# Kernel optimization log

Hardware: AMD Instinct MI355X
Metric: run time of the kernel (lower is better)

The kernel has to match this reference:

```python
import jax, jax.numpy as jnp
import numpy as np

DIM = 384
HEADS = 6
HEAD_DIM = DIM // HEADS
SCALE = HEAD_DIM ** -0.5
B = 16
HW = 56
NUM_TOKENS = 49


def _layernorm(x, g, b, eps):
    m = x.mean(-1, keepdims=True)
    v = ((x - m) ** 2).mean(-1, keepdims=True)
    return (x - m) * jax.lax.rsqrt(v + eps) * g + b


def _avgpool2(x):  # [B,C,H,W] -> [B,C,H/2,W/2], AvgPool2d(2,2)
    Bx, C, H, W = x.shape
    return x.reshape(Bx, C, H // 2, 2, W // 2, 2).mean(axis=(3, 5))


def _mha(q, k, v):  # q [B,Nq,C], k/v [B,Nk,C] -> [B,Nq,C]
    Bx, Nq, C = q.shape
    Nk = k.shape[1]
    qh = q.reshape(Bx, Nq, HEADS, HEAD_DIM).transpose(0, 2, 1, 3) * SCALE
    kh = k.reshape(Bx, Nk, HEADS, HEAD_DIM).transpose(0, 2, 1, 3)
    vh = v.reshape(Bx, Nk, HEADS, HEAD_DIM).transpose(0, 2, 1, 3)
    attn = jax.nn.softmax(jnp.einsum('bhqd,bhkd->bhqk', qh, kh), axis=-1)
    out = jnp.einsum('bhqk,bhkd->bhqd', attn, vh)
    return out.transpose(0, 2, 1, 3).reshape(Bx, Nq, C)


def setup_inputs() -> dict:
    key = jax.random.key(0)
    ks = jax.random.split(key, 16)
    s = 0.02
    return {
        'x': jax.random.normal(ks[0], (B, HW * HW, DIM), jnp.float32),
        'global_token': jax.random.normal(ks[1], (B, NUM_TOKENS, DIM), jnp.float32),
        # ConvEncoder (wsas[0]) params; linear weights stored [in,out] (= torch W.T)
        'we_dw_w': jax.random.normal(ks[2], (DIM, 1, 3, 3), jnp.float32) * 0.1,
        'we_dw_b': jnp.zeros((DIM,), jnp.float32),
        'we_ln_g': jnp.ones((DIM,), jnp.float32),
        'we_ln_b': jnp.zeros((DIM,), jnp.float32),
        'we_pw1_w': jax.random.normal(ks[3], (DIM, 4 * DIM), jnp.float32) * s,
        'we_pw1_b': jnp.zeros((4 * DIM,), jnp.float32),
        'we_pw2_w': jax.random.normal(ks[4], (4 * DIM, DIM), jnp.float32) * s,
        'we_pw2_b': jnp.zeros((DIM,), jnp.float32),
        'we_gamma': jnp.full((DIM,), 1e-6, jnp.float32),
        # ConvBNReLU (wsas[1]) params
        'cb_conv_w': jax.random.normal(ks[5], (DIM, DIM, 3, 3), jnp.float32) * s,
        'cb_ln_g': jnp.ones((DIM,), jnp.float32),
        'cb_ln_b': jnp.zeros((DIM,), jnp.float32),
        # attention projections (qkv_bias=False)
        'ga_qkv_w': jax.random.normal(ks[6], (DIM, 3 * DIM), jnp.float32) * s,
        'ug_kv_w': jax.random.normal(ks[7], (DIM, 2 * DIM), jnp.float32) * s,
        'ug_q_w': jax.random.normal(ks[8], (DIM, DIM), jnp.float32) * s,
        'gb_kv_w': jax.random.normal(ks[9], (DIM, 2 * DIM), jnp.float32) * s,
        'gb_q_w': jax.random.normal(ks[10], (DIM, DIM), jnp.float32) * s,
        'proj_w': jax.random.normal(ks[11], (DIM, DIM), jnp.float32) * s,
        'proj_b': jnp.zeros((DIM,), jnp.float32),
        'H': HW,
        'W': HW,
    }


def reference(x, global_token, we_dw_w, we_dw_b, we_ln_g, we_ln_b, we_pw1_w, we_pw1_b, we_pw2_w, we_pw2_b, we_gamma, cb_conv_w, cb_ln_g, cb_ln_b, ga_qkv_w, ug_kv_w, ug_q_w, gb_kv_w, gb_q_w, proj_w, proj_b, H, W):
    Bx, N, C = x.shape
    x_origin = x
    xc = x.reshape(Bx, H, W, C).transpose(0, 3, 1, 2)  # NCHW
    res = xc
    y = jax.lax.conv_general_dilated(xc, we_dw_w, (1, 1), 'SAME', feature_group_count=C, dimension_numbers=('NCHW', 'OIHW', 'NCHW')) + we_dw_b[None, :, None, None]
    y = y.transpose(0, 2, 3, 1)  # NHWC
    y = _layernorm(y, we_ln_g, we_ln_b, 1e-6)
    y = jax.nn.gelu(y @ we_pw1_w + we_pw1_b, approximate=False)
    y = (y @ we_pw2_w + we_pw2_b) * we_gamma
    xc = res + y.transpose(0, 3, 1, 2)
    x_local = xc.reshape(Bx, C, N).transpose(0, 2, 1)  # multi-scale[0]
    xc = _avgpool2(xc)  # down_1
    # --- wsas[1]: ConvBNReLU (3x3 conv, no bias + LN + ReLU) ---
    y = jax.lax.conv_general_dilated(xc, cb_conv_w, (1, 1), 'SAME', dimension_numbers=('NCHW', 'OIHW', 'NCHW'))
    y = _layernorm(y.transpose(0, 2, 3, 1), cb_ln_g, cb_ln_b, 1e-5)
    xc = jax.nn.relu(y).transpose(0, 3, 1, 2)
    xc = _avgpool2(xc)  # down_2 -> [B,C,14,14]
    xd = xc.reshape(Bx, C, -1).transpose(0, 2, 1)  # [B,196,C]
    # --- global aggregation: MHSA over downsampled tokens ---
    q, k, v = jnp.split(xd @ ga_qkv_w, 3, axis=-1)
    x_ds = _mha(q, k, v)
    # --- global token update: q = global tokens, kv = downsampled tokens ---
    k2, v2 = jnp.split(x_ds @ ug_kv_w, 2, axis=-1)
    gt = _mha(global_token @ ug_q_w, k2, v2)
    # --- global broadcast: q = image tokens, kv = global tokens ---
    k3, v3 = jnp.split(gt @ gb_kv_w, 2, axis=-1)
    x_global = _mha(x_origin @ gb_q_w, k3, v3)
    x_out = (x_local + x_global) @ proj_w + proj_b
    return x_out, gt
```

## Files before the change

### kernel.cpp

```cpp
#include <hip/hip_runtime.h>
#include <hip/hip_bf16.h>
#include <math.h>

#define DIM   384
#define HEADS 6
#define HD    64
#define NB    16
#define HW    56
#define N1    (HW*HW)
#define H2    28
#define N2    (H2*H2)
#define H3    14
#define N3    (H3*H3)
#define NT    49
#define HIDN  1536
#define SCL   0.125f
#define PH    30
#define PW    36

typedef short s8v __attribute__((ext_vector_type(8)));
typedef float f4v __attribute__((ext_vector_type(4)));

__device__ __forceinline__ short f2b(float f){
    unsigned u = __builtin_bit_cast(unsigned, f);
    unsigned r = (u + 0x7FFFu + ((u >> 16) & 1u)) >> 16;
    return (short)r;
}
__device__ __forceinline__ float b2f(short s){
    return __builtin_bit_cast(float, ((unsigned)(unsigned short)s) << 16);
}

__global__ void k_wconv(const float* __restrict__ w, short* __restrict__ wtb, int total)
{
    int idx = blockIdx.x * 256 + threadIdx.x;
    if (idx >= total) return;
    int ci  = idx % DIM;
    int tap = (idx / DIM) % 9;
    int co  = idx / (9*DIM);
    wtb[idx] = f2b(w[((size_t)co*DIM + ci)*9 + tap]);
}

__global__ __launch_bounds__(256)
void k_tcvt(const float* __restrict__ src, short* __restrict__ dst, int R, int C, int rt)
{
    int tile = blockIdx.x;
    int tr = tile % rt, tc = tile / rt;
    int r0 = tr*32, c0 = tc*32;
    int tx = threadIdx.x & 31, ty = threadIdx.x >> 5;
    __shared__ float t[32][33];
    #pragma unroll
    for (int j = 0; j < 4; ++j)
        t[ty + j*8][tx] = src[(size_t)(r0 + ty + j*8)*C + c0 + tx];
    __syncthreads();
    #pragma unroll
    for (int j = 0; j < 4; ++j)
        dst[(size_t)(c0 + ty + j*8)*R + r0 + tx] = f2b(t[tx][ty + j*8]);
}

__global__ __launch_bounds__(384)
void k_dwln(const float* __restrict__ x, const float* __restrict__ dww,
            const float* __restrict__ dwb, const float* __restrict__ g,
            const float* __restrict__ bt, short* __restrict__ out)
{
    const int pix = blockIdx.x;
    const int b = pix / N1, n = pix % N1;
    const int h = n / HW, w = n % HW;
    const int c = threadIdx.x;
    float acc = dwb[c];
    #pragma unroll
    for (int kh = 0; kh < 3; ++kh){
        int ih = h + kh - 1; if (ih < 0 || ih >= HW) continue;
        #pragma unroll
        for (int kw = 0; kw < 3; ++kw){
            int iw = w + kw - 1; if (iw < 0 || iw >= HW) continue;
            acc += x[((size_t)(b*N1 + ih*HW + iw))*DIM + c] * dww[c*9 + kh*3 + kw];
        }
    }
    float s = acc, q = acc*acc;
    #pragma unroll
    for (int off = 32; off; off >>= 1){ s += __shfl_down(s, off); q += __shfl_down(q, off); }
    __shared__ float rs[6], rq[6];
    int lane = threadIdx.x & 63, wv = threadIdx.x >> 6;
    if (!lane){ rs[wv] = s; rq[wv] = q; }
    __syncthreads();
    float ts = 0.f, tq = 0.f;
    #pragma unroll
    for (int i = 0; i < 6; ++i){ ts += rs[i]; tq += rq[i]; }
    float mean = ts * (1.f/DIM);
    float var  = tq * (1.f/DIM) - mean*mean;
    float rstd = rsqrtf(var + 1e-6f);
    out[(size_t)pix*DIM + c] = f2b((acc - mean) * rstd * g[c] + bt[c]);
}

#define XS_STR 392
#define HS_STR 72
__global__ __launch_bounds__(256)
void k_mlp_mfma(const short* __restrict__ xb, const float* __restrict__ x,
                const short* __restrict__ w1t, const float* __restrict__ b1,
                const short* __restrict__ w2t, const float* __restrict__ b2,
                const float* __restrict__ gamma, float* __restrict__ out)
{
    __shared__ short Xs[64*XS_STR];
    __shared__ short Hs[64*HS_STR];
    const int t0  = blockIdx.x * 64;
    const int tid = threadIdx.x;
    const int w   = tid >> 6;
    const int l   = tid & 63;
    const int lr  = l & 15;
    const int lg  = l >> 4;

    #pragma unroll
    for (int it = 0; it < 12; ++it){
        int i = tid + it*256;
        int row = i / 48, c8 = (i % 48) * 8;
        *(s8v*)&Xs[row*XS_STR + c8] = *(const s8v*)&xb[(size_t)(t0+row)*DIM + c8];
    }
    __syncthreads();

    f4v a2[4][6];
    #pragma unroll
    for (int m = 0; m < 4; ++m)
        #pragma unroll
        for (int n = 0; n < 6; ++n) a2[m][n] = (f4v){0.f,0.f,0.f,0.f};

    for (int ch = 0; ch < 24; ++ch){
        const int hc0 = ch * 64;
        f4v a1[4];
        #pragma unroll
        for (int m = 0; m < 4; ++m) a1[m] = (f4v){0.f,0.f,0.f,0.f};
        const int col1 = w*16 + lr;
        #pragma unroll 4
        for (int ks = 0; ks < 12; ++ks){
            const int k0 = ks*32 + lg*8;
            s8v bv = *(const s8v*)&w1t[(size_t)(hc0 + col1)*DIM + k0];
            #pragma unroll
            for (int m = 0; m < 4; ++m){
                s8v av = *(const s8v*)&Xs[(m*16 + lr)*XS_STR + k0];
                a1[m] = __builtin_amdgcn_mfma_f32_16x16x32_bf16(av, bv, a1[m], 0, 0, 0);
            }
        }
        float bb1 = b1[hc0 + col1];
        #pragma unroll
        for (int m = 0; m < 4; ++m){
            #pragma unroll
            for (int r = 0; r < 4; ++r){
                float h = a1[m][r] + bb1;
                float gl = h / (1.f + __expf(-1.702f * h));
                Hs[(m*16 + lg*4 + r)*HS_STR + col1] = f2b(gl);
            }
        }
        __syncthreads();
        #pragma unroll
        for (int ks = 0; ks < 2; ++ks){
            const int k0 = ks*32 + lg*8;
            s8v av[4];
            #pragma unroll
            for (int m = 0; m < 4; ++m)
                av[m] = *(const s8v*)&Hs[(m*16 + lr)*HS_STR + k0];
            #pragma unroll
            for (int n = 0; n < 6; ++n){
                s8v bv = *(const s8v*)&w2t[(size_t)(w*96 + n*16 + lr)*HIDN + hc0 + k0];
                #pragma unroll
                for (int m = 0; m < 4; ++m)
                    a2[m][n] = __builtin_amdgcn_mfma_f32_16x16x32_bf16(av[m], bv, a2[m][n], 0, 0, 0);
            }
        }
        __syncthreads();
    }
    #pragma unroll
    for (int n = 0; n < 6; ++n){
        const int col = w*96 + n*16 + lr;
        const float gm = gamma[col], bb2 = b2[col];
        #pragma unroll
        for (int m = 0; m < 4; ++m){
            #pragma unroll
            for (int r = 0; r < 4; ++r){
                size_t idx = (size_t)(t0 + m*16 + lg*4 + r)*DIM + col;
                out[idx] = x[idx] + gm * (a2[m][n][r] + bb2);
            }
        }
    }
}

__global__ __launch_bounds__(256)
void k_gemm_mfma(const float* __restrict__ A, const short* __restrict__ WT,
                 const float* __restrict__ bias, float* __restrict__ outf,
                 short* __restrict__ outb, int ldo)
{
    __shared__ short As[64*XS_STR];
    const int t0   = blockIdx.x * 64;
    const int col0 = blockIdx.y * 384;
    const int tid = threadIdx.x;
    const int w   = tid >> 6;
    const int l   = tid & 63;
    const int lr  = l & 15;
    const int lg  = l >> 4;

    #pragma unroll
    for (int it = 0; it < 12; ++it){
        int i = tid + it*256;
        int row = i / 48, c8 = (i % 48) * 8;
        const float4* p = (const float4*)&A[(size_t)(t0+row)*DIM + c8];
        float4 u = p[0], v = p[1];
        s8v pk;
        pk[0]=f2b(u.x); pk[1]=f2b(u.y); pk[2]=f2b(u.z); pk[3]=f2b(u.w);
        pk[4]=f2b(v.x); pk[5]=f2b(v.y); pk[6]=f2b(v.z); pk[7]=f2b(v.w);
        *(s8v*)&As[row*XS_STR + c8] = pk;
    }
    __syncthreads();

    f4v a2[4][6];
    #pragma unroll
    for (int m = 0; m < 4; ++m)
        #pragma unroll
        for (int n = 0; n < 6; ++n) a2[m][n] = (f4v){0.f,0.f,0.f,0.f};

    #pragma unroll 4
    for (int ks = 0; ks < 12; ++ks){
        const int k0 = ks*32 + lg*8;
        s8v av[4];
        #pragma unroll
        for (int m = 0; m < 4; ++m)
            av[m] = *(const s8v*)&As[(m*16 + lr)*XS_STR + k0];
        #pragma unroll
        for (int n = 0; n < 6; ++n){
            s8v bv = *(const s8v*)&WT[(size_t)(col0 + w*96 + n*16 + lr)*DIM + k0];
            #pragma unroll
            for (int m = 0; m < 4; ++m)
                a2[m][n] = __builtin_amdgcn_mfma_f32_16x16x32_bf16(av[m], bv, a2[m][n], 0, 0, 0);
        }
    }
    #pragma unroll
    for (int n = 0; n < 6; ++n){
        const int col = col0 + w*96 + n*16 + lr;
        const float bb = bias ? bias[col] : 0.f;
        #pragma unroll
        for (int m = 0; m < 4; ++m){
            #pragma unroll
            for (int r = 0; r < 4; ++r){
                size_t idx = (size_t)(t0 + m*16 + lg*4 + r)*ldo + col;
                float v = a2[m][n][r] + bb;
                if (outb) outb[idx] = f2b(v);
                else      outf[idx] = v;
            }
        }
    }
}

__global__ __launch_bounds__(384)
void k_poolpad(const float* __restrict__ in, short* __restrict__ pad)
{
    int pix = blockIdx.x;
    int b = pix / N2, r = pix % N2;
    int oh = r / H2, ow = r % H2;
    int c = threadIdx.x;
    size_t base = ((size_t)b * HW * HW + (size_t)(2*oh)*HW + 2*ow) * DIM;
    const float* p00 = &in[base];
    const float* p01 = p00 + DIM;
    const float* p10 = p00 + (size_t)HW*DIM;
    const float* p11 = p10 + DIM;
    float v = 0.25f * (p00[c] + p01[c] + p10[c] + p11[c]);
    pad[(((size_t)b*PH + oh + 1)*PW + ow + 1)*DIM + c] = f2b(v);
}

__global__ __launch_bounds__(256)
void k_conv_mfma(const short* __restrict__ pad, const short* __restrict__ wtb,
                 float* __restrict__ out)
{
    const int bx = blockIdx.x;
    const int oh = bx % H2;
    const int b  = bx / H2;
    const int tid = threadIdx.x;
    const int w   = tid >> 6;
    const int l   = tid & 63;
    const int lr  = l & 15;
    const int lg  = l >> 4;

    f4v acc[2][6];
    #pragma unroll
    for (int m = 0; m < 2; ++m)
        #pragma unroll
        for (int n = 0; n < 6; ++n) acc[m][n] = (f4v){0.f,0.f,0.f,0.f};

    #pragma unroll
    for (int kh = 0; kh < 3; ++kh){
        #pragma unroll
        for (int kw = 0; kw < 3; ++kw){
            const short* Ab = pad + (((size_t)b*PH + oh + kh)*PW + kw)*DIM;
            const short* Bb = wtb + (size_t)(kh*3 + kw)*DIM;
            #pragma unroll 3
            for (int ks = 0; ks < 12; ++ks){
                const int k0 = ks*32 + lg*8;
                s8v a0 = *(const s8v*)&Ab[(size_t)(lr     )*DIM + k0];
                s8v a1 = *(const s8v*)&Ab[(size_t)(lr + 16)*DIM + k0];
                #pragma unroll
                for (int n = 0; n < 6; ++n){
                    s8v bv = *(const s8v*)&Bb[(size_t)(w*96 + n*16 + lr)*(9*DIM) + k0];
                    acc[0][n] = __builtin_amdgcn_mfma_f32_16x16x32_bf16(a0, bv, acc[0][n], 0, 0, 0);
                    acc[1][n] = __builtin_amdgcn_mfma_f32_16x16x32_bf16(a1, bv, acc[1][n], 0, 0, 0);
                }
            }
        }
    }
    #pragma unroll
    for (int n = 0; n < 6; ++n){
        const int col = w*96 + n*16 + lr;
        #pragma unroll
        for (int m = 0; m < 2; ++m){
            #pragma unroll
            for (int r = 0; r < 4; ++r){
                int px = m*16 + lg*4 + r;
                if (px < H2)
                    out[((size_t)(b*N2 + oh*H2 + px))*DIM + col] = acc[m][n][r];
            }
        }
    }
}

__global__ __launch_bounds__(384)
void k_lnpool(const float* __restrict__ conv, const float* __restrict__ g,
              const float* __restrict__ bt, float* __restrict__ out)
{
    int pix = blockIdx.x;
    int b = pix / N3, r = pix % N3;
    int oh = r / H3, ow = r % H3;
    int c = threadIdx.x;
    float v[4];
    #pragma unroll
    for (int j = 0; j < 4; ++j){
        int ih = 2*oh + (j >> 1), iw = 2*ow + (j & 1);
        v[j] = conv[((size_t)(b*N2 + ih*H2 + iw))*DIM + c];
    }
    float s[4], q[4];
    #pragma unroll
    for (int j = 0; j < 4; ++j){ s[j] = v[j]; q[j] = v[j]*v[j]; }
    #pragma unroll
    for (int off = 32; off; off >>= 1){
        #pragma unroll
        for (int j = 0; j < 4; ++j){
            s[j] += __shfl_down(s[j], off);
            q[j] += __shfl_down(q[j], off);
        }
    }
    __shared__ float rs[6][4], rq[6][4];
    int lane = threadIdx.x & 63, wv = threadIdx.x >> 6;
    if (!lane){
        #pragma unroll
        for (int j = 0; j < 4; ++j){ rs[wv][j] = s[j]; rq[wv][j] = q[j]; }
    }
    __syncthreads();
    float gc = g[c], bc = bt[c];
    float o = 0.f;
    #pragma unroll
    for (int j = 0; j < 4; ++j){
        float ts = 0.f, tq = 0.f;
        #pragma unroll
        for (int i = 0; i < 6; ++i){ ts += rs[i][j]; tq += rq[i][j]; }
        float mean = ts * (1.f/DIM);
        float var  = tq * (1.f/DIM) - mean*mean;
        float rstd = rsqrtf(var + 1e-5f);
        o += fmaxf((v[j] - mean) * rstd * gc + bc, 0.f);
    }
    out[(size_t)pix*DIM + c] = 0.25f * o;
}

__global__ __launch_bounds__(256)
void k_gemm(const float* __restrict__ A, int lda,
            const float* __restrict__ W, const float* __restrict__ bias,
            float* __restrict__ out, int ldo, int K, int nb)
{
    int bx = blockIdx.x;
    int m0 = (bx / nb) * 16;
    int cb = (bx % nb) * 64;
    int tid = threadIdx.x;
    int r  = tid >> 4;
    int cg = tid & 15;
    int N  = nb * 64;
    __shared__ float As[16*32];
    __shared__ float Ws[32*64];
    float acc[4] = {0,0,0,0};
    for (int k0 = 0; k0 < K; k0 += 32){
        int e = tid;
        #pragma unroll
        for (int i = 0; i < 2; ++i){
            int rr = e >> 5, kk = e & 31;
            As[rr*32 + kk] = A[(size_t)(m0+rr)*lda + k0 + kk];
            e += 256;
        }
        int f = tid;
        #pragma unroll
        for (int i = 0; i < 8; ++i){
            int kr = f >> 6, cc = f & 63;
            Ws[kr*64 + cc] = W[(size_t)(k0+kr)*N + cb + cc];
            f += 256;
        }
        __syncthreads();
        #pragma unroll 8
        for (int kk = 0; kk < 32; ++kk){
            float a = As[r*32 + kk];
            #pragma unroll
            for (int j = 0; j < 4; ++j)
                acc[j] += a * Ws[kk*64 + cg*4 + j];
        }
        __syncthreads();
    }
    #pragma unroll
    for (int j = 0; j < 4; ++j){
        int c = cb + cg*4 + j;
        float v = acc[j] + (bias ? bias[c] : 0.f);
        out[(size_t)(m0 + r)*ldo + c] = v;
    }
}

__global__ __launch_bounds__(256)
void k_attn(const float* __restrict__ qp, const short* __restrict__ qb16, int ldq,
            const float* __restrict__ kp, const float* __restrict__ vp, int ldkv,
            float* __restrict__ op, int ldo,
            const float* __restrict__ addp,
            int Nq, int Nk, int qtiles)
{
    int bx = blockIdx.x;
    int qt = bx % qtiles;
    int h  = (bx / qtiles) % HEADS;
    int b  = bx / (qtiles * HEADS);
    int q0 = qt * 32;
    const float* kb = kp + (size_t)b*Nk*ldkv + h*HD;
    const float* vb = vp + (size_t)b*Nk*ldkv + h*HD;
    int tid = threadIdx.x;
    __shared__ float Q[32*HD];
    __shared__ float S[32*196];
    for (int e = tid; e < 32*HD; e += 256){
        int r = e >> 6, d = e & 63;
        float qv = 0.f;
        if (q0 + r < Nq){
            size_t qi = (size_t)(b*Nq + q0 + r)*ldq + h*HD + d;
            qv = (qb16 ? b2f(qb16[qi]) : qp[qi]) * SCL;
        }
        Q[e] = qv;
    }
    __syncthreads();
    for (int s = tid; s < 32*Nk; s += 256){
        int qi = s / Nk, ki = s - qi*Nk;
        if (q0 + qi < Nq){
            const float* kr = &kb[(size_t)ki*ldkv];
            float dot = 0.f;
            #pragma unroll 16
            for (int d = 0; d < HD; ++d) dot += Q[qi*HD + d] * kr[d];
            S[qi*196 + ki] = dot;
        }
    }
    __syncthreads();
    {
        int r = tid >> 3, sub = tid & 7;
        if (q0 + r < Nq){
            float m = -1e30f;
            for (int k = sub; k < Nk; k += 8) m = fmaxf(m, S[r*196 + k]);
            #pragma unroll
            for (int off = 4; off; off >>= 1) m = fmaxf(m, __shfl_xor(m, off, 8));
            float sum = 0.f;
            for (int k = sub; k < Nk; k += 8){
                float e = __expf(S[r*196 + k] - m);
                S[r*196 + k] = e;
                sum += e;
            }
            #pragma unroll
            for (int off = 4; off; off >>= 1) sum += __shfl_xor(sum, off, 8);
            float inv = 1.f / sum;
            for (int k = sub; k < Nk; k += 8) S[r*196 + k] *= inv;
        }
    }
    __syncthreads();
    {
        int qi = tid >> 3, d0 = (tid & 7) * 8;
        if (q0 + qi < Nq){
            float o[8] = {0,0,0,0,0,0,0,0};
            for (int k = 0; k < Nk; ++k){
                float p = S[qi*196 + k];
                const float* vr = &vb[(size_t)k*ldkv + d0];
                #pragma unroll
                for (int j = 0; j < 8; ++j) o[j] += p * vr[j];
            }
            size_t ob = (size_t)(b*Nq + q0 + qi)*ldo + h*HD + d0;
            #pragma unroll
            for (int j = 0; j < 8; ++j){
                float v = o[j];
                if (addp) v += addp[ob + j];
                op[ob + j] = v;
            }
        }
    }
}

extern "C" void kernel_launch(void* const* d_in, const int* in_sizes, int n_in,
                              void* d_out, int out_size, void* d_ws, size_t ws_size,
                              hipStream_t stream)
{
    const float* x    = (const float*)d_in[0];
    const float* gtok = (const float*)d_in[1];
    const float* dww  = (const float*)d_in[2];
    const float* dwb  = (const float*)d_in[3];
    const float* lng  = (const float*)d_in[4];
    const float* lnb  = (const float*)d_in[5];
    const float* w1   = (const float*)d_in[6];
    const float* b1   = (const float*)d_in[7];
    const float* w2   = (const float*)d_in[8];
    const float* b2   = (const float*)d_in[9];
    const float* gma  = (const float*)d_in[10];
    const float* cbw  = (const float*)d_in[11];
    const float* cbg  = (const float*)d_in[12];
    const float* cbb  = (const float*)d_in[13];
    const float* qkvw = (const float*)d_in[14];
    const float* ugkv = (const float*)d_in[15];
    const float* ugq  = (const float*)d_in[16];
    const float* gbkv = (const float*)d_in[17];
    const float* gbq  = (const float*)d_in[18];
    const float* pw   = (const float*)d_in[19];
    const float* pb   = (const float*)d_in[20];

    float* ws      = (float*)d_ws;
    float* xloc    = ws;
    float* convout = xloc    + (size_t)NB*N1*DIM;
    float* xd      = convout + (size_t)NB*N2*DIM;
    float* qkv     = xd      + (size_t)NB*N3*DIM;
    float* xds     = qkv     + (size_t)NB*N3*3*DIM;
    float* k2v2    = xds     + (size_t)NB*N3*DIM;
    float* gq      = k2v2    + (size_t)NB*N3*2*DIM;
    float* k3v3    = gq      + (size_t)NB*NT*DIM;
    short* xb      = (short*)(k3v3 + (size_t)NB*NT*2*DIM);
    short* pad1    = xb    + (size_t)NB*N1*DIM;
    short* wtb     = pad1  + (size_t)NB*PH*PW*DIM;
    short* w1t     = wtb   + (size_t)DIM*9*DIM;
    short* w2t     = w1t   + (size_t)HIDN*DIM;
    short* qkvwT   = w2t   + (size_t)DIM*HIDN;
    short* ugkvT   = qkvwT + (size_t)3*DIM*DIM;
    short* gbqT    = ugkvT + (size_t)2*DIM*DIM;
    short* pwT     = gbqT  + (size_t)DIM*DIM;
    short* q3b     = xb;

    float* xout = (float*)d_out;
    float* gt   = xout + (size_t)NB*N1*DIM;

    k_wconv<<<(DIM*9*DIM + 255)/256, 256, 0, stream>>>(cbw, wtb, DIM*9*DIM);
    k_tcvt<<<(DIM/32)*(HIDN/32), 256, 0, stream>>>(w1, w1t, DIM, HIDN, DIM/32);
    k_tcvt<<<(HIDN/32)*(DIM/32), 256, 0, stream>>>(w2, w2t, HIDN, DIM, HIDN/32);
    k_tcvt<<<(DIM/32)*(3*DIM/32), 256, 0, stream>>>(qkvw, qkvwT, DIM, 3*DIM, DIM/32);
    k_tcvt<<<(DIM/32)*(2*DIM/32), 256, 0, stream>>>(ugkv, ugkvT, DIM, 2*DIM, DIM/32);
    k_tcvt<<<(DIM/32)*(DIM/32), 256, 0, stream>>>(gbq, gbqT, DIM, DIM, DIM/32);
    k_tcvt<<<(DIM/32)*(DIM/32), 256, 0, stream>>>(pw, pwT, DIM, DIM, DIM/32);
    k_dwln<<<NB*N1, 384, 0, stream>>>(x, dww, dwb, lng, lnb, xb);
    k_mlp_mfma<<<NB*N1/64, 256, 0, stream>>>(xb, x, w1t, b1, w2t, b2, gma, xloc);
    hipMemsetAsync(pad1, 0, (size_t)NB*PH*PW*DIM*sizeof(short), stream);
    k_poolpad<<<NB*N2, 384, 0, stream>>>(xloc, pad1);
    k_conv_mfma<<<NB*H2, 256, 0, stream>>>(pad1, wtb, convout);
    k_lnpool<<<NB*N3, 384, 0, stream>>>(convout, cbg, cbb, xd);
    k_gemm_mfma<<<dim3(NB*N3/64, 3), 256, 0, stream>>>(xd, qkvwT, nullptr, qkv, nullptr, 3*DIM);
    k_attn<<<NB*HEADS*7, 256, 0, stream>>>(qkv, nullptr, 3*DIM, qkv+DIM, qkv+2*DIM, 3*DIM, xds, DIM, nullptr, N3, N3, 7);
    k_gemm_mfma<<<dim3(NB*N3/64, 2), 256, 0, stream>>>(xds, ugkvT, nullptr, k2v2, nullptr, 2*DIM);
    k_gemm<<<(NB*NT/16)*(DIM/64), 256, 0, stream>>>(gtok, DIM, ugq, nullptr, gq, DIM, DIM, DIM/64);
    k_attn<<<NB*HEADS*2, 256, 0, stream>>>(gq, nullptr, DIM, k2v2, k2v2+DIM, 2*DIM, gt, DIM, nullptr, NT, N3, 2);
    k_gemm<<<(NB*NT/16)*(2*DIM/64), 256, 0, stream>>>(gt, DIM, gbkv, nullptr, k3v3, 2*DIM, DIM, 2*DIM/64);
    k_gemm_mfma<<<dim3(NB*N1/64, 1), 256, 0, stream>>>(x, gbqT, nullptr, nullptr, q3b, DIM);
    k_attn<<<NB*HEADS*98, 256, 0, stream>>>(nullptr, q3b, DIM, k3v3, k3v3+DIM, 2*DIM, xloc, DIM, xloc, N1, NT, 98);
    k_gemm_mfma<<<dim3(NB*N1/64, 1), 256, 0, stream>>>(xloc, pwT, pb, xout, nullptr, DIM);
}
```

Before: 2.221 ms.

## Restructure MLP MFMA kernel, tile depthwise conv over pixels, vectorize attention loads

The MLP kernel now gives each wave 16 tokens, holds the X rows in registers, and computes the hidden layer in 32-wide chunks. The W2 chunks are double-buffered in shared memory through a register prefetch, so W2 is shared across waves instead of each wave reading it from global memory. The depthwise conv+LN kernel processes 4 horizontal pixels per block and reuses the loaded 3x6 window and weights. The attention kernel switches to float4 loads for QK and PV and takes a configurable score row stride, which is 56 for the 49-key case. The trade-off is higher register pressure from 24 accumulators plus 12 X vectors, which may reduce occupancy.

```diff
diff --git a/kernel.cpp b/kernel.cpp
--- a/kernel.cpp
+++ b/kernel.cpp
@@ -29,6 +29,9 @@
 __device__ __forceinline__ float b2f(short s){
     return __builtin_bit_cast(float, ((unsigned)(unsigned short)s) << 16);
 }
+__device__ __forceinline__ unsigned pk2(float a, float b){
+    return (unsigned)(unsigned short)f2b(a) | ((unsigned)(unsigned short)f2b(b) << 16);
+}
 
 __global__ void k_wconv(const float* __restrict__ w, short* __restrict__ wtb, int total)
 {
@@ -62,126 +65,165 @@
             const float* __restrict__ dwb, const float* __restrict__ g,
             const float* __restrict__ bt, short* __restrict__ out)
 {
-    const int pix = blockIdx.x;
-    const int b = pix / N1, n = pix % N1;
-    const int h = n / HW, w = n % HW;
-    const int c = threadIdx.x;
-    float acc = dwb[c];
-    #pragma unroll
-    for (int kh = 0; kh < 3; ++kh){
-        int ih = h + kh - 1; if (ih < 0 || ih >= HW) continue;
-        #pragma unroll
-        for (int kw = 0; kw < 3; ++kw){
-            int iw = w + kw - 1; if (iw < 0 || iw >= HW) continue;
-            acc += x[((size_t)(b*N1 + ih*HW + iw))*DIM + c] * dww[c*9 + kh*3 + kw];
-        }
-    }
-    float s = acc, q = acc*acc;
-    #pragma unroll
-    for (int off = 32; off; off >>= 1){ s += __shfl_down(s, off); q += __shfl_down(q, off); }
-    __shared__ float rs[6], rq[6];
-    int lane = threadIdx.x & 63, wv = threadIdx.x >> 6;
-    if (!lane){ rs[wv] = s; rq[wv] = q; }
-    __syncthreads();
-    float ts = 0.f, tq = 0.f;
-    #pragma unroll
-    for (int i = 0; i < 6; ++i){ ts += rs[i]; tq += rq[i]; }
-    float mean = ts * (1.f/DIM);
-    float var  = tq * (1.f/DIM) - mean*mean;
-    float rstd = rsqrtf(var + 1e-6f);
-    out[(size_t)pix*DIM + c] = f2b((acc - mean) * rstd * g[c] + bt[c]);
-}
-
-#define XS_STR 392
-#define HS_STR 72
+    const int bx = blockIdx.x;
+    const int wq = bx % 14;
+    const int h  = (bx / 14) % HW;
+    const int b  = bx / (14*HW);
+    const int w0 = wq * 4;
+    const int c  = threadIdx.x;
+    float wv[9];
+    #pragma unroll
+    for (int t = 0; t < 9; ++t) wv[t] = dww[c*9 + t];
+    float vin[3][6];
+    #pragma unroll
+    for (int rr = 0; rr < 3; ++rr){
+        int ih = h + rr - 1;
+        #pragma unroll
+        for (int cc = 0; cc < 6; ++cc){
+            int iw = w0 + cc - 1;
+            vin[rr][cc] = (ih >= 0 && ih < HW && iw >= 0 && iw < HW)
+                        ? x[((size_t)(b*N1 + ih*HW + iw))*DIM + c] : 0.f;
+        }
+    }
+    float bb = dwb[c];
+    float acc[4];
+    #pragma unroll
+    for (int p = 0; p < 4; ++p){
+        float a = bb;
+        #pragma unroll
+        for (int kh = 0; kh < 3; ++kh)
+            #pragma unroll
+            for (int kw = 0; kw < 3; ++kw)
+                a += vin[kh][p + kw] * wv[kh*3 + kw];
+        acc[p] = a;
+    }
+    float s[4], q[4];
+    #pragma unroll
+    for (int p = 0; p < 4; ++p){ s[p] = acc[p]; q[p] = acc[p]*acc[p]; }
+    #pragma unroll
+    for (int off = 32; off; off >>= 1){
+        #pragma unroll
+        for (int p = 0; p < 4; ++p){
+            s[p] += __shfl_down(s[p], off);
+            q[p] += __shfl_down(q[p], off);
+        }
+    }
+    __shared__ float rs[6][4], rq[6][4];
+    int lane = threadIdx.x & 63, wv_ = threadIdx.x >> 6;
+    if (!lane){
+        #pragma unroll
+        for (int p = 0; p < 4; ++p){ rs[wv_][p] = s[p]; rq[wv_][p] = q[p]; }
+    }
+    __syncthreads();
+    float gc = g[c], bc = bt[c];
+    #pragma unroll
+    for (int p = 0; p < 4; ++p){
+        float ts = 0.f, tq = 0.f;
+        #pragma unroll
+        for (int i = 0; i < 6; ++i){ ts += rs[i][p]; tq += rq[i][p]; }
+        float mean = ts * (1.f/DIM);
+        float var  = tq * (1.f/DIM) - mean*mean;
+        float rstd = rsqrtf(var + 1e-6f);
+        out[((size_t)(b*N1 + h*HW + w0 + p))*DIM + c] = f2b((acc[p] - mean)*rstd*gc + bc);
+    }
+}
+
+#define W2P 40
 __global__ __launch_bounds__(256)
 void k_mlp_mfma(const short* __restrict__ xb, const float* __restrict__ x,
                 const short* __restrict__ w1t, const float* __restrict__ b1,
                 const short* __restrict__ w2t, const float* __restrict__ b2,
                 const float* __restrict__ gamma, float* __restrict__ out)
 {
-    __shared__ short Xs[64*XS_STR];
-    __shared__ short Hs[64*HS_STR];
-    const int t0  = blockIdx.x * 64;
+    __shared__ short W2c[2*384*W2P];
+    __shared__ short Hs[4*16*W2P];
     const int tid = threadIdx.x;
-    const int w   = tid >> 6;
-    const int l   = tid & 63;
-    const int lr  = l & 15;
-    const int lg  = l >> 4;
-
-    #pragma unroll
-    for (int it = 0; it < 12; ++it){
-        int i = tid + it*256;
-        int row = i / 48, c8 = (i % 48) * 8;
-        *(s8v*)&Xs[row*XS_STR + c8] = *(const s8v*)&xb[(size_t)(t0+row)*DIM + c8];
-    }
-    __syncthreads();
-
-    f4v a2[4][6];
-    #pragma unroll
-    for (int m = 0; m < 4; ++m)
-        #pragma unroll
-        for (int n = 0; n < 6; ++n) a2[m][n] = (f4v){0.f,0.f,0.f,0.f};
-
-    for (int ch = 0; ch < 24; ++ch){
-        const int hc0 = ch * 64;
-        f4v a1[4];
-        #pragma unroll
-        for (int m = 0; m < 4; ++m) a1[m] = (f4v){0.f,0.f,0.f,0.f};
-        const int col1 = w*16 + lr;
-        #pragma unroll 4
-        for (int ks = 0; ks < 12; ++ks){
-            const int k0 = ks*32 + lg*8;
-            s8v bv = *(const s8v*)&w1t[(size_t)(hc0 + col1)*DIM + k0];
-            #pragma unroll
-            for (int m = 0; m < 4; ++m){
-                s8v av = *(const s8v*)&Xs[(m*16 + lr)*XS_STR + k0];
-                a1[m] = __builtin_amdgcn_mfma_f32_16x16x32_bf16(av, bv, a1[m], 0, 0, 0);
-            }
-        }
-        float bb1 = b1[hc0 + col1];
-        #pragma unroll
-        for (int m = 0; m < 4; ++m){
-            #pragma unroll
-            for (int r = 0; r < 4; ++r){
-                float h = a1[m][r] + bb1;
-                float gl = h / (1.f + __expf(-1.702f * h));
-                Hs[(m*16 + lg*4 + r)*HS_STR + col1] = f2b(gl);
+    const int w  = tid >> 6;
+    const int l  = tid & 63;
+    const int lr = l & 15;
+    const int lg = l >> 4;
+    const int tw = blockIdx.x*64 + w*16;
+    short* hsw = &Hs[w*16*W2P];
+
+    s8v xr[12];
+    #pragma unroll
+    for (int ks = 0; ks < 12; ++ks)
+        xr[ks] = *(const s8v*)&xb[(size_t)(tw + lr)*DIM + ks*32 + lg*8];
+
+    f4v acc[24];
+    #pragma unroll
+    for (int n = 0; n < 24; ++n) acc[n] = (f4v){0.f,0.f,0.f,0.f};
+
+    s8v sreg[6];
+    #pragma unroll
+    for (int c = 0; c < 6; ++c){
+        int f = tid + c*256, n = f >> 2, k = (f & 3)*8;
+        sreg[c] = *(const s8v*)&w2t[(size_t)n*HIDN + k];
+    }
+    #pragma unroll
+    for (int c = 0; c < 6; ++c){
+        int f = tid + c*256, n = f >> 2, k = (f & 3)*8;
+        *(s8v*)&W2c[n*W2P + k] = sreg[c];
+    }
+    __syncthreads();
+
+    for (int hp = 0; hp < 48; ++hp){
+        const int hc0 = hp*32;
+        if (hp < 47){
+            #pragma unroll
+            for (int c = 0; c < 6; ++c){
+                int f = tid + c*256, n = f >> 2, k = (f & 3)*8;
+                sreg[c] = *(const s8v*)&w2t[(size_t)n*HIDN + hc0 + 32 + k];
+            }
+        }
+        #pragma unroll
+        for (int ht = 0; ht < 2; ++ht){
+            f4v a1 = (f4v){0.f,0.f,0.f,0.f};
+            #pragma unroll
+            for (int ks = 0; ks < 12; ++ks){
+                s8v av = *(const s8v*)&w1t[(size_t)(hc0 + ht*16 + lr)*DIM + ks*32 + lg*8];
+                a1 = __builtin_amdgcn_mfma_f32_16x16x32_bf16(av, xr[ks], a1, 0, 0, 0);
+            }
+            float4 bb = *(const float4*)&b1[hc0 + ht*16 + lg*4];
+            float h0 = a1[0] + bb.x, h1 = a1[1] + bb.y;
+            float h2 = a1[2] + bb.z, h3 = a1[3] + bb.w;
+            h0 = h0 / (1.f + __expf(-1.702f*h0));
+            h1 = h1 / (1.f + __expf(-1.702f*h1));
+            h2 = h2 / (1.f + __expf(-1.702f*h2));
+            h3 = h3 / (1.f + __expf(-1.702f*h3));
+            *(unsigned*)&hsw[lr*W2P + ht*16 + lg*4]     = pk2(h0, h1);
+            *(unsigned*)&hsw[lr*W2P + ht*16 + lg*4 + 2] = pk2(h2, h3);
+        }
+        const short* cur = &W2c[(hp & 1)*384*W2P];
+        s8v ha = *(const s8v*)&hsw[lr*W2P + lg*8];
+        #pragma unroll
+        for (int n = 0; n < 24; ++n){
+            s8v bv = *(const s8v*)&cur[(n*16 + lr)*W2P + lg*8];
+            acc[n] = __builtin_amdgcn_mfma_f32_16x16x32_bf16(ha, bv, acc[n], 0, 0, 0);
+        }
+        if (hp < 47){
+            short* nxt = &W2c[((hp + 1) & 1)*384*W2P];
+            #pragma unroll
+            for (int c = 0; c < 6; ++c){
+                int f = tid + c*256, n = f >> 2, k = (f & 3)*8;
+                *(s8v*)&nxt[n*W2P + k] = sreg[c];
             }
         }
         __syncthreads();
-        #pragma unroll
-        for (int ks = 0; ks < 2; ++ks){
-            const int k0 = ks*32 + lg*8;
-            s8v av[4];
-            #pragma unroll
-            for (int m = 0; m < 4; ++m)
-                av[m] = *(const s8v*)&Hs[(m*16 + lr)*HS_STR + k0];
-            #pragma unroll
-            for (int n = 0; n < 6; ++n){
-                s8v bv = *(const s8v*)&w2t[(size_t)(w*96 + n*16 + lr)*HIDN + hc0 + k0];
-                #pragma unroll
-                for (int m = 0; m < 4; ++m)
-                    a2[m][n] = __builtin_amdgcn_mfma_f32_16x16x32_bf16(av[m], bv, a2[m][n], 0, 0, 0);
-            }
-        }
-        __syncthreads();
-    }
-    #pragma unroll
-    for (int n = 0; n < 6; ++n){
-        const int col = w*96 + n*16 + lr;
+    }
+    #pragma unroll
+    for (int n = 0; n < 24; ++n){
+        const int col = n*16 + lr;
         const float gm = gamma[col], bb2 = b2[col];
         #pragma unroll
-        for (int m = 0; m < 4; ++m){
-            #pragma unroll
-            for (int r = 0; r < 4; ++r){
-                size_t idx = (size_t)(t0 + m*16 + lg*4 + r)*DIM + col;
-                out[idx] = x[idx] + gm * (a2[m][n][r] + bb2);
-            }
-        }
-    }
-}
-
+        for (int r = 0; r < 4; ++r){
+            size_t idx = (size_t)(tw + lg*4 + r)*DIM + col;
+            out[idx] = x[idx] + gm * (acc[n][r] + bb2);
+        }
+    }
+}
+
+#define XS_STR 392
 __global__ __launch_bounds__(256)
 void k_gemm_mfma(const float* __restrict__ A, const short* __restrict__ WT,
                  const float* __restrict__ bias, float* __restrict__ outf,
@@ -417,7 +459,7 @@
             const float* __restrict__ kp, const float* __restrict__ vp, int ldkv,
             float* __restrict__ op, int ldo,
             const float* __restrict__ addp,
-            int Nq, int Nk, int qtiles)
+            int Nq, int Nk, int qtiles, int spad)
 {
     int bx = blockIdx.x;
     int qt = bx % qtiles;
@@ -442,11 +484,15 @@
     for (int s = tid; s < 32*Nk; s += 256){
         int qi = s / Nk, ki = s - qi*Nk;
         if (q0 + qi < Nq){
-            const float* kr = &kb[(size_t)ki*ldkv];
+            const float4* q4 = (const float4*)&Q[qi*HD];
+            const float4* k4 = (const float4*)&kb[(size_t)ki*ldkv];
             float dot = 0.f;
-            #pragma unroll 16
-            for (int d = 0; d < HD; ++d) dot += Q[qi*HD + d] * kr[d];
-            S[qi*196 + ki] = dot;
+            #pragma unroll
+            for (int d4 = 0; d4 < 16; ++d4){
+                float4 a = q4[d4], bq = k4[d4];
+                dot += a.x*bq.x + a.y*bq.y + a.z*bq.z + a.w*bq.w;
+            }
+            S[qi*spad + ki] = dot;
         }
     }
     __syncthreads();
@@ -454,19 +500,19 @@
         int r = tid >> 3, sub = tid & 7;
         if (q0 + r < Nq){
             float m = -1e30f;
-            for (int k = sub; k < Nk; k += 8) m = fmaxf(m, S[r*196 + k]);
+            for (int k = sub; k < Nk; k += 8) m = fmaxf(m, S[r*spad + k]);
             #pragma unroll
             for (int off = 4; off; off >>= 1) m = fmaxf(m, __shfl_xor(m, off, 8));
             float sum = 0.f;
             for (int k = sub; k < Nk; k += 8){
-                float e = __expf(S[r*196 + k] - m);
-                S[r*196 + k] = e;
+                float e = __expf(S[r*spad + k] - m);
+                S[r*spad + k] = e;
                 sum += e;
             }
             #pragma unroll
             for (int off = 4; off; off >>= 1) sum += __shfl_xor(sum, off, 8);
             float inv = 1.f / sum;
-            for (int k = sub; k < Nk; k += 8) S[r*196 + k] *= inv;
+            for (int k = sub; k < Nk; k += 8) S[r*spad + k] *= inv;
         }
     }
     __syncthreads();
@@ -475,10 +521,12 @@
         if (q0 + qi < Nq){
             float o[8] = {0,0,0,0,0,0,0,0};
             for (int k = 0; k < Nk; ++k){
-                float p = S[qi*196 + k];
+                float p = S[qi*spad + k];
                 const float* vr = &vb[(size_t)k*ldkv + d0];
-                #pragma unroll
-                for (int j = 0; j < 8; ++j) o[j] += p * vr[j];
+                float4 v0 = *(const float4*)&vr[0];
+                float4 v1 = *(const float4*)&vr[4];
+                o[0] += p*v0.x; o[1] += p*v0.y; o[2] += p*v0.z; o[3] += p*v0.w;
+                o[4] += p*v1.x; o[5] += p*v1.y; o[6] += p*v1.z; o[7] += p*v1.w;
             }
             size_t ob = (size_t)(b*Nq + q0 + qi)*ldo + h*HD + d0;
             #pragma unroll
@@ -547,19 +595,19 @@
     k_tcvt<<<(DIM/32)*(2*DIM/32), 256, 0, stream>>>(ugkv, ugkvT, DIM, 2*DIM, DIM/32);
     k_tcvt<<<(DIM/32)*(DIM/32), 256, 0, stream>>>(gbq, gbqT, DIM, DIM, DIM/32);
     k_tcvt<<<(DIM/32)*(DIM/32), 256, 0, stream>>>(pw, pwT, DIM, DIM, DIM/32);
-    k_dwln<<<NB*N1, 384, 0, stream>>>(x, dww, dwb, lng, lnb, xb);
+    k_dwln<<<NB*HW*14, 384, 0, stream>>>(x, dww, dwb, lng, lnb, xb);
     k_mlp_mfma<<<NB*N1/64, 256, 0, stream>>>(xb, x, w1t, b1, w2t, b2, gma, xloc);
     hipMemsetAsync(pad1, 0, (size_t)NB*PH*PW*DIM*sizeof(short), stream);
     k_poolpad<<<NB*N2, 384, 0, stream>>>(xloc, pad1);
     k_conv_mfma<<<NB*H2, 256, 0, stream>>>(pad1, wtb, convout);
     k_lnpool<<<NB*N3, 384, 0, stream>>>(convout, cbg, cbb, xd);
     k_gemm_mfma<<<dim3(NB*N3/64, 3), 256, 0, stream>>>(xd, qkvwT, nullptr, qkv, nullptr, 3*DIM);
-    k_attn<<<NB*HEADS*7, 256, 0, stream>>>(qkv, nullptr, 3*DIM, qkv+DIM, qkv+2*DIM, 3*DIM, xds, DIM, nullptr, N3, N3, 7);
+    k_attn<<<NB*HEADS*7, 256, 0, stream>>>(qkv, nullptr, 3*DIM, qkv+DIM, qkv+2*DIM, 3*DIM, xds, DIM, nullptr, N3, N3, 7, 196);
     k_gemm_mfma<<<dim3(NB*N3/64, 2), 256, 0, stream>>>(xds, ugkvT, nullptr, k2v2, nullptr, 2*DIM);
     k_gemm<<<(NB*NT/16)*(DIM/64), 256, 0, stream>>>(gtok, DIM, ugq, nullptr, gq, DIM, DIM, DIM/64);
-    k_attn<<<NB*HEADS*2, 256, 0, stream>>>(gq, nullptr, DIM, k2v2, k2v2+DIM, 2*DIM, gt, DIM, nullptr, NT, N3, 2);
+    k_attn<<<NB*HEADS*2, 256, 0, stream>>>(gq, nullptr, DIM, k2v2, k2v2+DIM, 2*DIM, gt, DIM, nullptr, NT, N3, 2, 196);
     k_gemm<<<(NB*NT/16)*(2*DIM/64), 256, 0, stream>>>(gt, DIM, gbkv, nullptr, k3v3, 2*DIM, DIM, 2*DIM/64);
     k_gemm_mfma<<<dim3(NB*N1/64, 1), 256, 0, stream>>>(x, gbqT, nullptr, nullptr, q3b, DIM);
-    k_attn<<<NB*HEADS*98, 256, 0, stream>>>(nullptr, q3b, DIM, k3v3, k3v3+DIM, 2*DIM, xloc, DIM, xloc, N1, NT, 98);
+    k_attn<<<NB*HEADS*98, 256, 0, stream>>>(nullptr, q3b, DIM, k3v3, k3v3+DIM, 2*DIM, xloc, DIM, xloc, N1, NT, 98, 56);
     k_gemm_mfma<<<dim3(NB*N1/64, 1), 256, 0, stream>>>(xloc, pwT, pb, xout, nullptr, DIM);
 }
```

Measured after the change: 2.265 ms. No clear change (+2.0%).
